# Optimization experiments

Hardware: AMD Instinct MI355X
Metric: run time of the kernel (lower is better)

Reference implementation:

```python
import jax, jax.numpy as jnp
import numpy as np

B, T, C = 1, 2048, 1024
H, KVH = 16, 4
D = C // H            # 64
KV = KVH * D          # 256
EPS = 1e-6
SCALE = 1.0 / np.sqrt(D)
ROPE_BASE = 10000.0


def setup_inputs() -> dict:
    key = jax.random.key(0)
    ks = jax.random.split(key, 8)
    s = 0.02
    return dict(
        x=jax.random.normal(ks[0], (B, T, C), jnp.float32),
        Wq=jax.random.normal(ks[1], (C, C), jnp.float32) * s,
        Wk=jax.random.normal(ks[2], (KV, C), jnp.float32) * s,
        Wv=jax.random.normal(ks[3], (KV, C), jnp.float32) * s,
        Wo=jax.random.normal(ks[4], (C, C), jnp.float32) * s,
        q_norm_w=jnp.ones((C,), jnp.float32),
        k_norm_w=jnp.ones((KV,), jnp.float32),
        fgate_w=jax.random.normal(ks[5], (H, C), jnp.float32) * s,
        fgate_b=jnp.zeros((H,), jnp.float32),
        weight_lambda=jax.random.normal(ks[6], (C, H), jnp.float32) * s,
    )


def _rmsnorm(x, w):
    var = jnp.mean(x * x, axis=-1, keepdims=True)
    return x * jax.lax.rsqrt(var + EPS) * w


def _rotate_half(x):
    x1, x2 = jnp.split(x, 2, axis=-1)
    return jnp.concatenate([-x2, x1], axis=-1)


def _apply_rope(q, k):
    # q: [B,H,T,D], k: [B,KVH,T,D]; position_ids = arange(T)
    inv_freq = 1.0 / (ROPE_BASE ** (jnp.arange(0, D, 2, dtype=jnp.float32) / D))
    freqs = jnp.outer(jnp.arange(T, dtype=jnp.float32), inv_freq)  # [T, D/2]
    emb = jnp.concatenate([freqs, freqs], axis=-1)                 # [T, D]
    cos = jnp.cos(emb)[None, None]                                  # [1,1,T,D]
    sin = jnp.sin(emb)[None, None]
    return q * cos + _rotate_half(q) * sin, k * cos + _rotate_half(k) * sin


def _forward(x, Wq, Wk, Wv, Wo, q_norm_w, k_norm_w, fgate_w, fgate_b, weight_lambda):
    q = _rmsnorm(x @ Wq.T, q_norm_w)          # [B,T,C]
    k = _rmsnorm(x @ Wk.T, k_norm_w)          # [B,T,KV]
    v = x @ Wv.T                              # [B,T,KV]
    q = q.reshape(B, T, H, D).transpose(0, 2, 1, 3)     # [B,H,T,D]
    k = k.reshape(B, T, KVH, D).transpose(0, 2, 1, 3)   # [B,KVH,T,D]
    v = v.reshape(B, T, KVH, D).transpose(0, 2, 1, 3)
    q, k = _apply_rope(q, k)
    # GQA: repeat_interleave kv heads
    g = H // KVH
    k = jnp.repeat(k, g, axis=1)              # [B,H,T,D]
    v = jnp.repeat(v, g, axis=1)
    # Forgetting gate (FoX): log f_t per head, with elu-based lambda scaling
    lam = jax.nn.elu(x @ weight_lambda) + 1.0            # [B,T,H]
    logit = (x @ fgate_w.T + fgate_b) * lam              # [B,T,H]
    log_f = (jax.nn.log_sigmoid(logit) / (lam + 1e-3)).transpose(0, 2, 1)  # [B,H,T]
    c = jnp.cumsum(log_f, axis=-1)                       # [B,H,T]
    bias = c[..., :, None] - c[..., None, :]             # [B,H,T,T]: sum_{t=j+1..i} log f_t
    scores = jnp.einsum('bhid,bhjd->bhij', q, k) * SCALE + bias
    causal = jnp.tril(jnp.ones((T, T), dtype=bool))
    scores = jnp.where(causal, scores, -jnp.inf)
    p = jax.nn.softmax(scores, axis=-1)
    y = jnp.einsum('bhij,bhjd->bhid', p, v)              # [B,H,T,D]
    y = y.transpose(0, 2, 1, 3).reshape(B, T, C)
    return y @ Wo.T


def reference(x, Wq, Wk, Wv, Wo, q_norm_w, k_norm_w, fgate_w, fgate_b, weight_lambda):
    return _forward(x, Wq, Wk, Wv, Wo, q_norm_w, k_norm_w, fgate_w, fgate_b, weight_lambda)
```

## Files before the change

kernel.cpp:

```cpp
#include <hip/hip_runtime.h>

typedef __bf16 bf16x8 __attribute__((ext_vector_type(8)));
typedef float f32x4 __attribute__((ext_vector_type(4)));

#define MFMA_BF16 __builtin_amdgcn_mfma_f32_16x16x32_bf16

static constexpr int T_ = 2048;
static constexpr int C_ = 1024;
static constexpr int H_ = 16;
static constexpr int KVH_ = 4;
static constexpr int D_ = 64;
static constexpr float SCALE_ = 0.125f;
static constexpr float MSHIFT_ = 10.0f;

__device__ inline void cvt8(__bf16* dst, const float* src) {
  float4 a = *(const float4*)src;
  float4 b = *(const float4*)(src + 4);
  bf16x8 r;
  r[0] = (__bf16)a.x; r[1] = (__bf16)a.y; r[2] = (__bf16)a.z; r[3] = (__bf16)a.w;
  r[4] = (__bf16)b.x; r[5] = (__bf16)b.y; r[6] = (__bf16)b.z; r[7] = (__bf16)b.w;
  *(bf16x8*)dst = r;
}

__global__ __launch_bounds__(256) void cvt_kernel(
    const float* __restrict__ x,  const float* __restrict__ wq,
    const float* __restrict__ wk, const float* __restrict__ wv,
    const float* __restrict__ wo, const float* __restrict__ wl,
    __bf16* __restrict__ xb,  __bf16* __restrict__ wqb,
    __bf16* __restrict__ wkb, __bf16* __restrict__ wvb,
    __bf16* __restrict__ wob, float* __restrict__ wlT,
    float* __restrict__ zbuf)
{
  size_t i8 = ((size_t)blockIdx.x * 256 + threadIdx.x) * 8;
  if (i8 < 2097152)       cvt8(xb  + i8,            x  + i8);
  else if (i8 < 3145728)  cvt8(wqb + (i8-2097152),  wq + (i8-2097152));
  else if (i8 < 3407872)  cvt8(wkb + (i8-3145728),  wk + (i8-3145728));
  else if (i8 < 3670016)  cvt8(wvb + (i8-3407872),  wv + (i8-3407872));
  else if (i8 < 4718592)  cvt8(wob + (i8-3670016),  wo + (i8-3670016));
  else if (i8 < 4734976) {
    size_t r = i8 - 4718592;
#pragma unroll
    for (int j = 0; j < 8; ++j) {
      size_t idx = r + j;
      size_t hh = idx >> 10, c = idx & 1023;
      wlT[idx] = wl[c * 16 + hh];
    }
  } else {
    size_t z = i8 - 4734976;
    if (z < 2129920) {
      float4 zz = {0.f, 0.f, 0.f, 0.f};
      *(float4*)(zbuf + z) = zz;
      *(float4*)(zbuf + z + 4) = zz;
    }
  }
}

template <int BM>
__global__ __launch_bounds__(256) void gemm_bt_kernel(
    const __bf16* __restrict__ A, int K, int N,
    const __bf16* __restrict__ B0, int e0,
    const __bf16* __restrict__ B1, int e1,
    const __bf16* __restrict__ B2,
    float* __restrict__ outF)
{
  __shared__ __bf16 la[BM * 40];
  __shared__ __bf16 lb[128 * 40];
  const int m0 = blockIdx.y * BM;
  const int n0 = blockIdx.x * 128;
  const __bf16* Bs; int nrel;
  if (n0 < e0)      { Bs = B0; nrel = n0; }
  else if (n0 < e1) { Bs = B1; nrel = n0 - e0; }
  else              { Bs = B2; nrel = n0 - e1; }
  const int tid = threadIdx.x;
  const int arow = tid >> 2, acol = (tid & 3) * 8;
  const __bf16* ap = A  + (size_t)(m0   + arow) * K + acol;
  const __bf16* bp = Bs + (size_t)(nrel + arow) * K + acol;
  const int w = tid >> 6, lane = tid & 63, lq = lane >> 4, ln = lane & 15;
  const int wm = (w >> 1) * (BM / 2), wn = (w & 1) * 64;
  constexpr int FM = BM / 32;
  f32x4 acc[FM][4] = {};
  for (int k0 = 0; k0 < K; k0 += 32) {
    bf16x8 a0 = *(const bf16x8*)(ap + k0);
    bf16x8 a1{};
    if (BM == 128) a1 = *(const bf16x8*)(ap + (size_t)64 * K + k0);
    bf16x8 b0 = *(const bf16x8*)(bp + k0);
    bf16x8 b1 = *(const bf16x8*)(bp + (size_t)64 * K + k0);
    __syncthreads();
    *(bf16x8*)(la + arow * 40 + acol) = a0;
    if (BM == 128) *(bf16x8*)(la + (arow + 64) * 40 + acol) = a1;
    *(bf16x8*)(lb + arow * 40 + acol) = b0;
    *(bf16x8*)(lb + (arow + 64) * 40 + acol) = b1;
    __syncthreads();
    bf16x8 af[FM], bfr[4];
#pragma unroll
    for (int i = 0; i < FM; ++i)
      af[i] = *(const bf16x8*)(la + (wm + i * 16 + ln) * 40 + lq * 8);
#pragma unroll
    for (int j = 0; j < 4; ++j)
      bfr[j] = *(const bf16x8*)(lb + (wn + j * 16 + ln) * 40 + lq * 8);
#pragma unroll
    for (int i = 0; i < FM; ++i)
#pragma unroll
      for (int j = 0; j < 4; ++j)
        acc[i][j] = MFMA_BF16(af[i], bfr[j], acc[i][j], 0, 0, 0);
  }
#pragma unroll
  for (int i = 0; i < FM; ++i)
#pragma unroll
    for (int j = 0; j < 4; ++j)
#pragma unroll
      for (int r = 0; r < 4; ++r) {
        int row = m0 + wm + i * 16 + lq * 4 + r;
        int col = n0 + wn + j * 16 + ln;
        outF[(size_t)row * N + col] = acc[i][j][r];
      }
}

__global__ __launch_bounds__(256) void gates_kernel(
    const float* __restrict__ x, const float* __restrict__ fw,
    const float* __restrict__ fb, const float* __restrict__ wlT,
    float* __restrict__ logf)
{
  const int t = blockIdx.x;
  const int tid = threadIdx.x, w = tid >> 6, lane = tid & 63;
  float xv[16];
#pragma unroll
  for (int i = 0; i < 16; ++i)
    xv[i] = x[(size_t)t * C_ + i * 64 + lane];
#pragma unroll
  for (int u = 0; u < 4; ++u) {
    int h = w * 4 + u;
    float s1 = 0.f, s2 = 0.f;
#pragma unroll
    for (int i = 0; i < 16; ++i) {
      int cidx = i * 64 + lane;
      s1 += xv[i] * wlT[(size_t)h * C_ + cidx];
      s2 += xv[i] * fw[(size_t)h * C_ + cidx];
    }
    for (int m = 32; m; m >>= 1) {
      s1 += __shfl_xor(s1, m);
      s2 += __shfl_xor(s2, m);
    }
    if (lane == 0) {
      float lam = (s1 > 0.f ? s1 : expm1f(s1)) + 1.0f;
      float logit = (s2 + fb[h]) * lam;
      float ls = (logit >= 0.f) ? -log1pf(expf(-logit))
                                : (logit - log1pf(expf(logit)));
      logf[(size_t)h * T_ + t] = ls / (lam + 1e-3f);
    }
  }
}

__global__ __launch_bounds__(64) void cumsum_kernel(
    const float* __restrict__ logf, float* __restrict__ csum)
{
  const int h = blockIdx.x;
  const int lane = threadIdx.x;
  float carry = 0.f;
  for (int ch = 0; ch < T_ / 64; ++ch) {
    float v = logf[(size_t)h * T_ + ch * 64 + lane];
#pragma unroll
    for (int d = 1; d < 64; d <<= 1) {
      float tv = __shfl_up(v, d);
      if (lane >= d) v += tv;
    }
    v += carry;
    csum[(size_t)h * T_ + ch * 64 + lane] = v;
    carry = __shfl(v, 63);
  }
}

__global__ __launch_bounds__(256) void normrope_kernel(
    const float* __restrict__ qkv, const float* __restrict__ qw,
    const float* __restrict__ kw, __bf16* __restrict__ qh,
    __bf16* __restrict__ kh, __bf16* __restrict__ vh)
{
  const int t = blockIdx.x, tid = threadIdx.x;
  __shared__ float qn[1024];
  __shared__ float kn[256];
  __shared__ float red[16];
  __shared__ float rc[32], rs[32];
  if (tid < 32) {
    float fr = (float)t * exp2f((float)tid * -0.41524101186404527f);
    float sn, cs;
    sincosf(fr, &sn, &cs);
    rc[tid] = cs; rs[tid] = sn;
  }
  const float* row = qkv + (size_t)t * 1536;
  float4 q4 = *(const float4*)(row + tid * 4);
  float kvl = row[1024 + tid];
  float vvl = row[1280 + tid];
  float ssq = q4.x * q4.x + q4.y * q4.y + q4.z * q4.z + q4.w * q4.w;
  float ssk = kvl * kvl;
  const int lane = tid & 63, w = tid >> 6;
  for (int m = 32; m; m >>= 1) {
    ssq += __shfl_xor(ssq, m);
    ssk += __shfl_xor(ssk, m);
  }
  if (lane == 0) { red[w] = ssq; red[8 + w] = ssk; }
  __syncthreads();
  float sq = red[0] + red[1] + red[2] + red[3];
  float sk = red[8] + red[9] + red[10] + red[11];
  float rq = rsqrtf(sq * (1.0f / 1024.f) + 1e-6f);
  float rk = rsqrtf(sk * (1.0f / 256.f) + 1e-6f);
  qn[tid * 4 + 0] = q4.x * rq * qw[tid * 4 + 0];
  qn[tid * 4 + 1] = q4.y * rq * qw[tid * 4 + 1];
  qn[tid * 4 + 2] = q4.z * rq * qw[tid * 4 + 2];
  qn[tid * 4 + 3] = q4.w * rq * qw[tid * 4 + 3];
  kn[tid] = kvl * rk * kw[tid];
  __syncthreads();
#pragma unroll
  for (int u = 0; u < 4; ++u) {
    int cidx = tid * 4 + u;
    int hh = cidx >> 6, d = cidx & 63, i = d & 31;
    float cs = rc[i], sn = rs[i];
    float val = (d < 32) ? (qn[cidx] * cs - qn[cidx + 32] * sn)
                         : (qn[cidx] * cs + qn[cidx - 32] * sn);
    qh[(size_t)hh * T_ * D_ + (size_t)t * D_ + d] = (__bf16)val;
  }
  {
    int d = tid & 63, kvhh = tid >> 6, i = d & 31;
    float cs = rc[i], sn = rs[i];
    float kval = (d < 32) ? (kn[tid] * cs - kn[tid + 32] * sn)
                          : (kn[tid] * cs + kn[tid - 32] * sn);
    kh[(size_t)kvhh * T_ * D_ + (size_t)t * D_ + d] = (__bf16)kval;
    vh[(size_t)kvhh * T_ * D_ + (size_t)t * D_ + d] = (__bf16)vvl;
  }
}

__global__ __launch_bounds__(256) void vtrans_kernel(
    const __bf16* __restrict__ vh, __bf16* __restrict__ vt)
{
  const int tb = blockIdx.x, kvh = blockIdx.y;
  __shared__ __bf16 tile[64][72];
  const int tid = threadIdx.x;
  const int r = tid >> 2, cb = (tid & 3) * 16;
  const __bf16* src = vh + (size_t)kvh * T_ * D_ + (size_t)(tb * 64 + r) * D_ + cb;
  bf16x8 v0 = *(const bf16x8*)(src);
  bf16x8 v1 = *(const bf16x8*)(src + 8);
  *(bf16x8*)(&tile[r][cb]) = v0;
  *(bf16x8*)(&tile[r][cb + 8]) = v1;
  __syncthreads();
  bf16x8 o0, o1;
#pragma unroll
  for (int j = 0; j < 8; ++j) o0[j] = tile[cb + j][r];
#pragma unroll
  for (int j = 0; j < 8; ++j) o1[j] = tile[cb + 8 + j][r];
  __bf16* dst = vt + (size_t)kvh * D_ * T_ + (size_t)r * T_ + tb * 64 + cb;
  *(bf16x8*)(dst) = o0;
  *(bf16x8*)(dst + 8) = o1;
}

__global__ __launch_bounds__(256) void attn_kernel(
    const __bf16* __restrict__ qh, const __bf16* __restrict__ kh,
    const __bf16* __restrict__ vt, const float* __restrict__ csum,
    __bf16* __restrict__ y, float* __restrict__ oacc,
    float* __restrict__ lsacc)
{
  const int ib = blockIdx.x, h = blockIdx.y, sg = blockIdx.z;
  const int jt0 = sg * 8;
  if (jt0 > ib) return;
  const int i0 = ib * 64, kvh = h >> 2;
  const int jtend = min(jt0 + 8, ib);
  const bool hasdiag = ((ib >> 3) == sg);
  const int nseg = (ib >> 3) + 1;
  __shared__ __bf16 kt[64 * 72];
  __shared__ __bf16 vtt[64 * 72];
  __shared__ __bf16 pt[4][16 * 72];
  const int tid = threadIdx.x;
  const int w = tid >> 6, lane = tid & 63, lq = lane >> 4, ln = lane & 15;
  const int srow = tid >> 2, scol = (tid & 3) * 16;
  const __bf16* kbase = kh + (size_t)kvh * T_ * D_;
  const __bf16* vbase = vt + (size_t)kvh * D_ * T_;
  const __bf16* qp = qh + ((size_t)h * T_ + i0 + w * 16 + ln) * D_;
  bf16x8 aq0 = *(const bf16x8*)(qp + lq * 8);
  bf16x8 aq1 = *(const bf16x8*)(qp + 32 + lq * 8);
  float ci[4];
#pragma unroll
  for (int r = 0; r < 4; ++r)
    ci[r] = csum[(size_t)h * T_ + i0 + w * 16 + lq * 4 + r];
  f32x4 o[4] = {};
  f32x4 ls = {0.f, 0.f, 0.f, 0.f};
  bf16x8 ones;
#pragma unroll
  for (int j = 0; j < 8; ++j) ones[j] = (__bf16)1.0f;
  __bf16* pw = &pt[w][0];

  bf16x8 kr0 = *(const bf16x8*)(kbase + (size_t)(jt0 * 64 + srow) * D_ + scol);
  bf16x8 kr1 = *(const bf16x8*)(kbase + (size_t)(jt0 * 64 + srow) * D_ + scol + 8);
  bf16x8 vr0 = *(const bf16x8*)(vbase + (size_t)srow * T_ + jt0 * 64 + scol);
  bf16x8 vr1 = *(const bf16x8*)(vbase + (size_t)srow * T_ + jt0 * 64 + scol + 8);
  *(bf16x8*)(kt + srow * 72 + scol) = kr0;
  *(bf16x8*)(kt + srow * 72 + scol + 8) = kr1;
  *(bf16x8*)(vtt + srow * 72 + scol) = vr0;
  *(bf16x8*)(vtt + srow * 72 + scol + 8) = vr1;
  __syncthreads();

  auto tilebody = [&](int j0, bool diag) {
    f32x4 s[4];
    const f32x4 zf = {0.f, 0.f, 0.f, 0.f};
#pragma unroll
    for (int jj = 0; jj < 4; ++jj) {
      bf16x8 bk0 = *(const bf16x8*)(kt + (jj * 16 + ln) * 72 + lq * 8);
      bf16x8 bk1 = *(const bf16x8*)(kt + (jj * 16 + ln) * 72 + 32 + lq * 8);
      s[jj] = MFMA_BF16(aq0, bk0, zf, 0, 0, 0);
      s[jj] = MFMA_BF16(aq1, bk1, s[jj], 0, 0, 0);
    }
    float cj[4];
#pragma unroll
    for (int jj = 0; jj < 4; ++jj)
      cj[jj] = csum[(size_t)h * T_ + j0 + jj * 16 + ln];
#pragma unroll
    for (int jj = 0; jj < 4; ++jj)
#pragma unroll
      for (int r = 0; r < 4; ++r) {
        float arg = fmaf(s[jj][r], SCALE_, ci[r] - cj[jj] - MSHIFT_);
        float p = __expf(arg);
        if (diag && (jj * 16 + ln > w * 16 + lq * 4 + r)) p = 0.f;
        pw[(lq * 4 + r) * 72 + jj * 16 + ln] = (__bf16)p;
      }
    asm volatile("s_waitcnt lgkmcnt(0)" ::: "memory");
    bf16x8 pa0 = *(const bf16x8*)(pw + ln * 72 + lq * 8);
    bf16x8 pa1 = *(const bf16x8*)(pw + ln * 72 + 32 + lq * 8);
    ls = MFMA_BF16(pa0, ones, ls, 0, 0, 0);
    ls = MFMA_BF16(pa1, ones, ls, 0, 0, 0);
#pragma unroll
    for (int dd = 0; dd < 4; ++dd) {
      bf16x8 bv0 = *(const bf16x8*)(vtt + (dd * 16 + ln) * 72 + lq * 8);
      bf16x8 bv1 = *(const bf16x8*)(vtt + (dd * 16 + ln) * 72 + 32 + lq * 8);
      o[dd] = MFMA_BF16(pa0, bv0, o[dd], 0, 0, 0);
      o[dd] = MFMA_BF16(pa1, bv1, o[dd], 0, 0, 0);
    }
  };

  for (int jt = jt0; jt < jtend; ++jt) {
    const bool pf = (jt + 1 < jtend) || hasdiag;
    const int j0n = (jt + 1) * 64;
    if (pf) {
      kr0 = *(const bf16x8*)(kbase + (size_t)(j0n + srow) * D_ + scol);
      kr1 = *(const bf16x8*)(kbase + (size_t)(j0n + srow) * D_ + scol + 8);
      vr0 = *(const bf16x8*)(vbase + (size_t)srow * T_ + j0n + scol);
      vr1 = *(const bf16x8*)(vbase + (size_t)srow * T_ + j0n + scol + 8);
    }
    tilebody(jt * 64, false);
    if (pf) {
      __syncthreads();
      *(bf16x8*)(kt + srow * 72 + scol) = kr0;
      *(bf16x8*)(kt + srow * 72 + scol + 8) = kr1;
      *(bf16x8*)(vtt + srow * 72 + scol) = vr0;
      *(bf16x8*)(vtt + srow * 72 + scol + 8) = vr1;
      __syncthreads();
    }
  }
  if (hasdiag) tilebody(i0, true);

  if (nseg == 1) {
#pragma unroll
    for (int dd = 0; dd < 4; ++dd)
#pragma unroll
      for (int r = 0; r < 4; ++r) {
        int iabs = i0 + w * 16 + lq * 4 + r;
        int col = h * 64 + dd * 16 + ln;
        y[(size_t)iabs * C_ + col] = (__bf16)(o[dd][r] / ls[r]);
      }
  } else {
#pragma unroll
    for (int dd = 0; dd < 4; ++dd)
#pragma unroll
      for (int r = 0; r < 4; ++r) {
        int iabs = i0 + w * 16 + lq * 4 + r;
        atomicAdd(oacc + ((size_t)h * T_ + iabs) * D_ + dd * 16 + ln, o[dd][r]);
      }
    if (ln == 0) {
#pragma unroll
      for (int r = 0; r < 4; ++r)
        atomicAdd(lsacc + (size_t)h * T_ + i0 + w * 16 + lq * 4 + r, ls[r]);
    }
  }
}

__global__ __launch_bounds__(256) void attnfin_kernel(
    const float* __restrict__ oacc, const float* __restrict__ lsacc,
    __bf16* __restrict__ y)
{
  const int t = 512 + blockIdx.x;
  const int c = threadIdx.x * 4;
  const int h = c >> 6, d = c & 63;
  float inv = 1.0f / lsacc[(size_t)h * T_ + t];
  float4 o4 = *(const float4*)(oacc + ((size_t)h * T_ + t) * D_ + d);
  __bf16* yp = y + (size_t)t * C_ + c;
  yp[0] = (__bf16)(o4.x * inv);
  yp[1] = (__bf16)(o4.y * inv);
  yp[2] = (__bf16)(o4.z * inv);
  yp[3] = (__bf16)(o4.w * inv);
}

extern "C" void kernel_launch(void* const* d_in, const int* in_sizes, int n_in,
                              void* d_out, int out_size, void* d_ws, size_t ws_size,
                              hipStream_t stream) {
  const float* x   = (const float*)d_in[0];
  const float* Wq  = (const float*)d_in[1];
  const float* Wk  = (const float*)d_in[2];
  const float* Wv  = (const float*)d_in[3];
  const float* Wo  = (const float*)d_in[4];
  const float* qnw = (const float*)d_in[5];
  const float* knw = (const float*)d_in[6];
  const float* fgw = (const float*)d_in[7];
  const float* fgb = (const float*)d_in[8];
  const float* wl  = (const float*)d_in[9];

  char* ws = (char*)d_ws;
  size_t off = 0;
  float*  qkv  = (float*)(ws + off);  off += (size_t)T_ * 1536 * 4;
  float*  logf = (float*)(ws + off);  off += (size_t)H_ * T_ * 4;
  float*  csum = (float*)(ws + off);  off += (size_t)H_ * T_ * 4;
  __bf16* qh   = (__bf16*)(ws + off); off += (size_t)H_ * T_ * D_ * 2;
  __bf16* kh   = (__bf16*)(ws + off); off += (size_t)KVH_ * T_ * D_ * 2;
  __bf16* vh   = (__bf16*)(ws + off); off += (size_t)KVH_ * T_ * D_ * 2;
  __bf16* vt   = (__bf16*)(ws + off); off += (size_t)KVH_ * T_ * D_ * 2;
  __bf16* y    = (__bf16*)(ws + off); off += (size_t)T_ * C_ * 2;
  __bf16* xb   = (__bf16*)(ws + off); off += (size_t)T_ * C_ * 2;
  __bf16* wqb  = (__bf16*)(ws + off); off += (size_t)C_ * C_ * 2;
  __bf16* wkb  = (__bf16*)(ws + off); off += (size_t)256 * C_ * 2;
  __bf16* wvb  = (__bf16*)(ws + off); off += (size_t)256 * C_ * 2;
  __bf16* wob  = (__bf16*)(ws + off); off += (size_t)C_ * C_ * 2;
  float*  wlT  = (float*)(ws + off);  off += (size_t)H_ * C_ * 4;
  float*  oacc = (float*)(ws + off);  off += (size_t)H_ * T_ * D_ * 4;
  float*  lsacc= (float*)(ws + off);  off += (size_t)H_ * T_ * 4;

  cvt_kernel<<<3352, 256, 0, stream>>>(x, Wq, Wk, Wv, Wo, wl,
                                       xb, wqb, wkb, wvb, wob, wlT, oacc);
  gemm_bt_kernel<64><<<dim3(12, 32), 256, 0, stream>>>(
      xb, 1024, 1536, wqb, 1024, wkb, 1280, wvb, qkv);
  gates_kernel<<<T_, 256, 0, stream>>>(x, fgw, fgb, wlT, logf);
  cumsum_kernel<<<H_, 64, 0, stream>>>(logf, csum);
  normrope_kernel<<<T_, 256, 0, stream>>>(qkv, qnw, knw, qh, kh, vh);
  vtrans_kernel<<<dim3(T_ / 64, KVH_), 256, 0, stream>>>(vh, vt);
  attn_kernel<<<dim3(T_ / 64, H_, 4), 256, 0, stream>>>(qh, kh, vt, csum, y,
                                                        oacc, lsacc);
  attnfin_kernel<<<T_ - 512, 256, 0, stream>>>(oacc, lsacc, y);
  gemm_bt_kernel<64><<<dim3(8, 32), 256, 0, stream>>>(
      y, 1024, 1024, wob, 1024, wob, 1024, wob, (float*)d_out);
}
```

Measured before the change: 203.2 us.

## Load K and V fragments directly from global memory, dropping LDS staging

The attention kernel no longer stages K and V tiles in shared memory with register prefetch and two barriers per tile. Each wave now reads its MFMA B-operand fragments for K and V straight from global memory, relying on the caches. This removes the barriers and the LDS write and read traffic. In exchange, the four waves each issue redundant global loads for the same tile, and the software prefetch that overlapped the next tile's load with compute is gone.

```diff
diff --git a/kernel.cpp b/kernel.cpp
--- a/kernel.cpp
+++ b/kernel.cpp
@@ -264,12 +264,9 @@
   const int jtend = min(jt0 + 8, ib);
   const bool hasdiag = ((ib >> 3) == sg);
   const int nseg = (ib >> 3) + 1;
-  __shared__ __bf16 kt[64 * 72];
-  __shared__ __bf16 vtt[64 * 72];
   __shared__ __bf16 pt[4][16 * 72];
   const int tid = threadIdx.x;
   const int w = tid >> 6, lane = tid & 63, lq = lane >> 4, ln = lane & 15;
-  const int srow = tid >> 2, scol = (tid & 3) * 16;
   const __bf16* kbase = kh + (size_t)kvh * T_ * D_;
   const __bf16* vbase = vt + (size_t)kvh * D_ * T_;
   const __bf16* qp = qh + ((size_t)h * T_ + i0 + w * 16 + ln) * D_;
@@ -286,30 +283,21 @@
   for (int j = 0; j < 8; ++j) ones[j] = (__bf16)1.0f;
   __bf16* pw = &pt[w][0];
 
-  bf16x8 kr0 = *(const bf16x8*)(kbase + (size_t)(jt0 * 64 + srow) * D_ + scol);
-  bf16x8 kr1 = *(const bf16x8*)(kbase + (size_t)(jt0 * 64 + srow) * D_ + scol + 8);
-  bf16x8 vr0 = *(const bf16x8*)(vbase + (size_t)srow * T_ + jt0 * 64 + scol);
-  bf16x8 vr1 = *(const bf16x8*)(vbase + (size_t)srow * T_ + jt0 * 64 + scol + 8);
-  *(bf16x8*)(kt + srow * 72 + scol) = kr0;
-  *(bf16x8*)(kt + srow * 72 + scol + 8) = kr1;
-  *(bf16x8*)(vtt + srow * 72 + scol) = vr0;
-  *(bf16x8*)(vtt + srow * 72 + scol + 8) = vr1;
-  __syncthreads();
-
   auto tilebody = [&](int j0, bool diag) {
+    float cj[4];
+#pragma unroll
+    for (int jj = 0; jj < 4; ++jj)
+      cj[jj] = csum[(size_t)h * T_ + j0 + jj * 16 + ln];
     f32x4 s[4];
     const f32x4 zf = {0.f, 0.f, 0.f, 0.f};
 #pragma unroll
     for (int jj = 0; jj < 4; ++jj) {
-      bf16x8 bk0 = *(const bf16x8*)(kt + (jj * 16 + ln) * 72 + lq * 8);
-      bf16x8 bk1 = *(const bf16x8*)(kt + (jj * 16 + ln) * 72 + 32 + lq * 8);
+      const __bf16* kr = kbase + (size_t)(j0 + jj * 16 + ln) * D_ + lq * 8;
+      bf16x8 bk0 = *(const bf16x8*)(kr);
+      bf16x8 bk1 = *(const bf16x8*)(kr + 32);
       s[jj] = MFMA_BF16(aq0, bk0, zf, 0, 0, 0);
       s[jj] = MFMA_BF16(aq1, bk1, s[jj], 0, 0, 0);
     }
-    float cj[4];
-#pragma unroll
-    for (int jj = 0; jj < 4; ++jj)
-      cj[jj] = csum[(size_t)h * T_ + j0 + jj * 16 + ln];
 #pragma unroll
     for (int jj = 0; jj < 4; ++jj)
 #pragma unroll
@@ -326,32 +314,16 @@
     ls = MFMA_BF16(pa1, ones, ls, 0, 0, 0);
 #pragma unroll
     for (int dd = 0; dd < 4; ++dd) {
-      bf16x8 bv0 = *(const bf16x8*)(vtt + (dd * 16 + ln) * 72 + lq * 8);
-      bf16x8 bv1 = *(const bf16x8*)(vtt + (dd * 16 + ln) * 72 + 32 + lq * 8);
+      const __bf16* vr = vbase + (size_t)(dd * 16 + ln) * T_ + j0 + lq * 8;
+      bf16x8 bv0 = *(const bf16x8*)(vr);
+      bf16x8 bv1 = *(const bf16x8*)(vr + 32);
       o[dd] = MFMA_BF16(pa0, bv0, o[dd], 0, 0, 0);
       o[dd] = MFMA_BF16(pa1, bv1, o[dd], 0, 0, 0);
     }
   };
 
-  for (int jt = jt0; jt < jtend; ++jt) {
-    const bool pf = (jt + 1 < jtend) || hasdiag;
-    const int j0n = (jt + 1) * 64;
-    if (pf) {
-      kr0 = *(const bf16x8*)(kbase + (size_t)(j0n + srow) * D_ + scol);
-      kr1 = *(const bf16x8*)(kbase + (size_t)(j0n + srow) * D_ + scol + 8);
-      vr0 = *(const bf16x8*)(vbase + (size_t)srow * T_ + j0n + scol);
-      vr1 = *(const bf16x8*)(vbase + (size_t)srow * T_ + j0n + scol + 8);
-    }
+  for (int jt = jt0; jt < jtend; ++jt)
     tilebody(jt * 64, false);
-    if (pf) {
-      __syncthreads();
-      *(bf16x8*)(kt + srow * 72 + scol) = kr0;
-      *(bf16x8*)(kt + srow * 72 + scol + 8) = kr1;
-      *(bf16x8*)(vtt + srow * 72 + scol) = vr0;
-      *(bf16x8*)(vtt + srow * 72 + scol + 8) = vr1;
-      __syncthreads();
-    }
-  }
   if (hasdiag) tilebody(i0, true);
 
   if (nseg == 1) {
```

Result: slower. 283.5 us (+39.5%).

## Share K/V tiles across GQA head group and shorten split-K segments

Applied to the files above, without the earlier changes.

Each attention block now handles one KV head, and its four warps each process a different query head over all 64 rows of the tile. The K/V tile loaded into shared memory is therefore reused by the four query heads, cutting K/V global and LDS fill traffic per query head. The key-range split shrinks from 8 to 4 tiles per segment, which doubles the grid depth to improve load balance. In exchange, per-warp register state and the per-warp P buffer grow, and occupancy is pinned with launch bounds of 2 blocks per CU. More partial results now go through atomic accumulation.

```diff
diff --git a/kernel.cpp b/kernel.cpp
--- a/kernel.cpp
+++ b/kernel.cpp
@@ -10,6 +10,7 @@
 static constexpr int H_ = 16;
 static constexpr int KVH_ = 4;
 static constexpr int D_ = 64;
+static constexpr int SEGT_ = 4;
 static constexpr float SCALE_ = 0.125f;
 static constexpr float MSHIFT_ = 10.0f;
 
@@ -251,36 +252,41 @@
   *(bf16x8*)(dst + 8) = o1;
 }
 
-__global__ __launch_bounds__(256) void attn_kernel(
+__global__ __launch_bounds__(256, 2) void attn_kernel(
     const __bf16* __restrict__ qh, const __bf16* __restrict__ kh,
     const __bf16* __restrict__ vt, const float* __restrict__ csum,
     __bf16* __restrict__ y, float* __restrict__ oacc,
     float* __restrict__ lsacc)
 {
-  const int ib = blockIdx.x, h = blockIdx.y, sg = blockIdx.z;
-  const int jt0 = sg * 8;
+  const int ib = blockIdx.x, kvh = blockIdx.y, sg = blockIdx.z;
+  const int jt0 = sg * SEGT_;
   if (jt0 > ib) return;
-  const int i0 = ib * 64, kvh = h >> 2;
-  const int jtend = min(jt0 + 8, ib);
-  const bool hasdiag = ((ib >> 3) == sg);
-  const int nseg = (ib >> 3) + 1;
+  const int i0 = ib * 64;
+  const int jtend = min(jt0 + SEGT_, ib);
+  const bool hasdiag = ((ib >> 2) == sg);
+  const int nseg = (ib >> 2) + 1;
   __shared__ __bf16 kt[64 * 72];
   __shared__ __bf16 vtt[64 * 72];
-  __shared__ __bf16 pt[4][16 * 72];
+  __shared__ __bf16 pt[4][64 * 76];
   const int tid = threadIdx.x;
   const int w = tid >> 6, lane = tid & 63, lq = lane >> 4, ln = lane & 15;
   const int srow = tid >> 2, scol = (tid & 3) * 16;
+  const int h = kvh * 4 + w;
   const __bf16* kbase = kh + (size_t)kvh * T_ * D_;
   const __bf16* vbase = vt + (size_t)kvh * D_ * T_;
-  const __bf16* qp = qh + ((size_t)h * T_ + i0 + w * 16 + ln) * D_;
-  bf16x8 aq0 = *(const bf16x8*)(qp + lq * 8);
-  bf16x8 aq1 = *(const bf16x8*)(qp + 32 + lq * 8);
-  float ci[4];
-#pragma unroll
-  for (int r = 0; r < 4; ++r)
-    ci[r] = csum[(size_t)h * T_ + i0 + w * 16 + lq * 4 + r];
-  f32x4 o[4] = {};
-  f32x4 ls = {0.f, 0.f, 0.f, 0.f};
+  bf16x8 aq0[4], aq1[4];
+  float ci[4][4];
+#pragma unroll
+  for (int i = 0; i < 4; ++i) {
+    const __bf16* qp = qh + ((size_t)h * T_ + i0 + i * 16 + ln) * D_;
+    aq0[i] = *(const bf16x8*)(qp + lq * 8);
+    aq1[i] = *(const bf16x8*)(qp + 32 + lq * 8);
+#pragma unroll
+    for (int r = 0; r < 4; ++r)
+      ci[i][r] = csum[(size_t)h * T_ + i0 + i * 16 + lq * 4 + r];
+  }
+  f32x4 o[4][4] = {};
+  f32x4 ls[4] = {};
   bf16x8 ones;
 #pragma unroll
   for (int j = 0; j < 8; ++j) ones[j] = (__bf16)1.0f;
@@ -297,39 +303,53 @@
   __syncthreads();
 
   auto tilebody = [&](int j0, bool diag) {
-    f32x4 s[4];
-    const f32x4 zf = {0.f, 0.f, 0.f, 0.f};
-#pragma unroll
-    for (int jj = 0; jj < 4; ++jj) {
-      bf16x8 bk0 = *(const bf16x8*)(kt + (jj * 16 + ln) * 72 + lq * 8);
-      bf16x8 bk1 = *(const bf16x8*)(kt + (jj * 16 + ln) * 72 + 32 + lq * 8);
-      s[jj] = MFMA_BF16(aq0, bk0, zf, 0, 0, 0);
-      s[jj] = MFMA_BF16(aq1, bk1, s[jj], 0, 0, 0);
-    }
     float cj[4];
 #pragma unroll
     for (int jj = 0; jj < 4; ++jj)
       cj[jj] = csum[(size_t)h * T_ + j0 + jj * 16 + ln];
-#pragma unroll
-    for (int jj = 0; jj < 4; ++jj)
-#pragma unroll
-      for (int r = 0; r < 4; ++r) {
-        float arg = fmaf(s[jj][r], SCALE_, ci[r] - cj[jj] - MSHIFT_);
-        float p = __expf(arg);
-        if (diag && (jj * 16 + ln > w * 16 + lq * 4 + r)) p = 0.f;
-        pw[(lq * 4 + r) * 72 + jj * 16 + ln] = (__bf16)p;
+    bf16x8 bk0[4], bk1[4];
+#pragma unroll
+    for (int jj = 0; jj < 4; ++jj) {
+      bk0[jj] = *(const bf16x8*)(kt + (jj * 16 + ln) * 72 + lq * 8);
+      bk1[jj] = *(const bf16x8*)(kt + (jj * 16 + ln) * 72 + 32 + lq * 8);
+    }
+    const f32x4 zf = {0.f, 0.f, 0.f, 0.f};
+#pragma unroll
+    for (int i = 0; i < 4; ++i) {
+      f32x4 s[4];
+#pragma unroll
+      for (int jj = 0; jj < 4; ++jj) {
+        s[jj] = MFMA_BF16(aq0[i], bk0[jj], zf, 0, 0, 0);
+        s[jj] = MFMA_BF16(aq1[i], bk1[jj], s[jj], 0, 0, 0);
       }
+#pragma unroll
+      for (int jj = 0; jj < 4; ++jj)
+#pragma unroll
+        for (int r = 0; r < 4; ++r) {
+          float arg = fmaf(s[jj][r], SCALE_, ci[i][r] - cj[jj] - MSHIFT_);
+          float p = __expf(arg);
+          if (diag && (jj * 16 + ln > i * 16 + lq * 4 + r)) p = 0.f;
+          pw[(i * 16 + lq * 4 + r) * 76 + jj * 16 + ln] = (__bf16)p;
+        }
+    }
     asm volatile("s_waitcnt lgkmcnt(0)" ::: "memory");
-    bf16x8 pa0 = *(const bf16x8*)(pw + ln * 72 + lq * 8);
-    bf16x8 pa1 = *(const bf16x8*)(pw + ln * 72 + 32 + lq * 8);
-    ls = MFMA_BF16(pa0, ones, ls, 0, 0, 0);
-    ls = MFMA_BF16(pa1, ones, ls, 0, 0, 0);
+    bf16x8 bv0[4], bv1[4];
 #pragma unroll
     for (int dd = 0; dd < 4; ++dd) {
-      bf16x8 bv0 = *(const bf16x8*)(vtt + (dd * 16 + ln) * 72 + lq * 8);
-      bf16x8 bv1 = *(const bf16x8*)(vtt + (dd * 16 + ln) * 72 + 32 + lq * 8);
-      o[dd] = MFMA_BF16(pa0, bv0, o[dd], 0, 0, 0);
-      o[dd] = MFMA_BF16(pa1, bv1, o[dd], 0, 0, 0);
+      bv0[dd] = *(const bf16x8*)(vtt + (dd * 16 + ln) * 72 + lq * 8);
+      bv1[dd] = *(const bf16x8*)(vtt + (dd * 16 + ln) * 72 + 32 + lq * 8);
+    }
+#pragma unroll
+    for (int i = 0; i < 4; ++i) {
+      bf16x8 pa0 = *(const bf16x8*)(pw + (i * 16 + ln) * 76 + lq * 8);
+      bf16x8 pa1 = *(const bf16x8*)(pw + (i * 16 + ln) * 76 + 32 + lq * 8);
+      ls[i] = MFMA_BF16(pa0, ones, ls[i], 0, 0, 0);
+      ls[i] = MFMA_BF16(pa1, ones, ls[i], 0, 0, 0);
+#pragma unroll
+      for (int dd = 0; dd < 4; ++dd) {
+        o[i][dd] = MFMA_BF16(pa0, bv0[dd], o[i][dd], 0, 0, 0);
+        o[i][dd] = MFMA_BF16(pa1, bv1[dd], o[i][dd], 0, 0, 0);
+      }
     }
   };
 
@@ -356,25 +376,33 @@
 
   if (nseg == 1) {
 #pragma unroll
-    for (int dd = 0; dd < 4; ++dd)
-#pragma unroll
-      for (int r = 0; r < 4; ++r) {
-        int iabs = i0 + w * 16 + lq * 4 + r;
-        int col = h * 64 + dd * 16 + ln;
-        y[(size_t)iabs * C_ + col] = (__bf16)(o[dd][r] / ls[r]);
-      }
+    for (int i = 0; i < 4; ++i)
+#pragma unroll
+      for (int dd = 0; dd < 4; ++dd)
+#pragma unroll
+        for (int r = 0; r < 4; ++r) {
+          int iabs = i0 + i * 16 + lq * 4 + r;
+          int col = h * 64 + dd * 16 + ln;
+          y[(size_t)iabs * C_ + col] = (__bf16)(o[i][dd][r] / ls[i][r]);
+        }
   } else {
 #pragma unroll
-    for (int dd = 0; dd < 4; ++dd)
-#pragma unroll
-      for (int r = 0; r < 4; ++r) {
-        int iabs = i0 + w * 16 + lq * 4 + r;
-        atomicAdd(oacc + ((size_t)h * T_ + iabs) * D_ + dd * 16 + ln, o[dd][r]);
-      }
+    for (int i = 0; i < 4; ++i)
+#pragma unroll
+      for (int dd = 0; dd < 4; ++dd)
+#pragma unroll
+        for (int r = 0; r < 4; ++r) {
+          int iabs = i0 + i * 16 + lq * 4 + r;
+          atomicAdd(oacc + ((size_t)h * T_ + iabs) * D_ + dd * 16 + ln,
+                    o[i][dd][r]);
+        }
     if (ln == 0) {
 #pragma unroll
-      for (int r = 0; r < 4; ++r)
-        atomicAdd(lsacc + (size_t)h * T_ + i0 + w * 16 + lq * 4 + r, ls[r]);
+      for (int i = 0; i < 4; ++i)
+#pragma unroll
+        for (int r = 0; r < 4; ++r)
+          atomicAdd(lsacc + (size_t)h * T_ + i0 + i * 16 + lq * 4 + r,
+                    ls[i][r]);
     }
   }
 }
@@ -383,7 +411,7 @@
     const float* __restrict__ oacc, const float* __restrict__ lsacc,
     __bf16* __restrict__ y)
 {
-  const int t = 512 + blockIdx.x;
+  const int t = SEGT_ * 64 + blockIdx.x;
   const int c = threadIdx.x * 4;
   const int h = c >> 6, d = c & 63;
   float inv = 1.0f / lsacc[(size_t)h * T_ + t];
@@ -436,9 +464,9 @@
   cumsum_kernel<<<H_, 64, 0, stream>>>(logf, csum);
   normrope_kernel<<<T_, 256, 0, stream>>>(qkv, qnw, knw, qh, kh, vh);
   vtrans_kernel<<<dim3(T_ / 64, KVH_), 256, 0, stream>>>(vh, vt);
-  attn_kernel<<<dim3(T_ / 64, H_, 4), 256, 0, stream>>>(qh, kh, vt, csum, y,
-                                                        oacc, lsacc);
-  attnfin_kernel<<<T_ - 512, 256, 0, stream>>>(oacc, lsacc, y);
+  attn_kernel<<<dim3(T_ / 64, KVH_, T_ / 64 / SEGT_), 256, 0, stream>>>(
+      qh, kh, vt, csum, y, oacc, lsacc);
+  attnfin_kernel<<<T_ - SEGT_ * 64, 256, 0, stream>>>(oacc, lsacc, y);
   gemm_bt_kernel<64><<<dim3(8, 32), 256, 0, stream>>>(
       y, 1024, 1024, wob, 1024, wob, 1024, wob, (float*)d_out);
 }
```

Result: slower. 220.7 us (+8.6%).
